# Performance work log

Hardware: AMD Instinct MI355X
Metric: run time of the kernel (lower is better)

The kernel has to match this reference:

```python
import jax, jax.numpy as jnp
import numpy as np


def setup_inputs() -> dict:
    key = jax.random.key(0)
    k0, k1, k2, k3 = jax.random.split(key, 4)
    B, in_dim, n_vars, out_dim, E = 64, 512, 512, 720, 8
    x = jax.random.normal(k0, (B, in_dim, n_vars), dtype=jnp.float32)
    # Gating: nn.Linear(in_dim, E, bias=False) -> weight [E, in_dim]
    Wg = jax.random.normal(k1, (E, in_dim), dtype=jnp.float32) * 0.02
    # Experts: nn.Linear(in_dim, out_dim) -> weight [out_dim, in_dim], bias [out_dim]
    We = jax.random.normal(k2, (E, out_dim, in_dim), dtype=jnp.float32) * 0.02
    be = jax.random.normal(k3, (E, out_dim), dtype=jnp.float32) * 0.02
    return {"x": x, "Wg": Wg, "We": We, "be": be, "top_k": 2}


def reference(x, Wg, We, be, top_k):
    # x: [B, in_len, n_vars] -> tokens along n_vars with feature dim in_len
    xt = jnp.swapaxes(x, 1, 2)                      # [B, V, D]
    gate = jax.nn.softmax(xt @ Wg.T, axis=-1)       # [B, V, E]
    weights, sel = jax.lax.top_k(gate, top_k)       # [B, V, k]
    E, O, D = We.shape
    out = jnp.zeros(xt.shape[:2] + (O,), dtype=xt.dtype)  # [B, V, O]
    for e in range(E):
        # combine weight for expert e: sum over top-k slots routed to e
        coef = jnp.sum(jnp.where(sel == e, weights, jnp.zeros_like(weights)), axis=-1)  # [B, V]
        out = out + coef[..., None] * (jnp.einsum('bvd,od->bvo', xt, We[e]) + be[e])
    return jnp.swapaxes(out, 1, 2)                  # [B, pred_len, n_vars]
```

## Files before the change

kernel.cpp:

```cpp
#include <hip/hip_runtime.h>
#include <hip/hip_bf16.h>

#define DID 512
#define NV  512
#define NB  64
#define OD  720
#define OPAD 768
#define NE  8
#define NTOK (NB * NV)
#define MAXTILE 512

typedef short  bf16x8 __attribute__((ext_vector_type(8)));
typedef float  f32x4  __attribute__((ext_vector_type(4)));

#define XT_OFF    0u
#define WB_OFF    33554432u
#define PID_OFF   39845888u
#define C1D_OFF   39976960u
#define C2D_OFF   40108032u
#define TL_OFF    40239104u
#define CL1_OFF   40370176u
#define CL2_OFF   40501248u
#define BCNT_OFF  40632320u
#define BFILL_OFF 40632576u
#define BOFF_OFF  40632832u
#define TPID_OFF  40633088u
#define TT0_OFF   40635136u
#define TEND_OFF  40637184u
#define NT_OFF    40639232u
#define SCR_OFF   40639488u
#define SCR_END   87825408u

static __device__ __forceinline__ ushort f2bf(float f) {
  unsigned u = __float_as_uint(f);
  unsigned r = (u + 0x7fffu + ((u >> 16) & 1u)) >> 16;
  return (ushort)r;
}
static __device__ __forceinline__ float bf2f(ushort u) {
  return __uint_as_float(((unsigned)u) << 16);
}
static __device__ __forceinline__ void async16(const ushort* g, ushort* l) {
  __builtin_amdgcn_global_load_lds((__attribute__((address_space(1))) void*)(g),
                                   (__attribute__((address_space(3))) void*)(l),
                                   16, 0, 0);
}
static __device__ __forceinline__ int swz(int r) { return (r & 3) ^ ((r >> 2) & 1); }

__global__ __launch_bounds__(512, 4) void k_gatet(const float* __restrict__ x,
                                                  const float* __restrict__ Wg,
                                                  ushort* __restrict__ xt,
                                                  int* __restrict__ pairid,
                                                  float* __restrict__ c1d,
                                                  float* __restrict__ c2d,
                                                  int* __restrict__ bcnt) {
  __shared__ float wg[NE * DID];
  __shared__ float part[8][64][NE + 1];
  __shared__ int cnt64[64];
  const int tid = threadIdx.x;
  for (int i = tid; i < NE * DID / 4; i += 512)
    ((float4*)wg)[i] = ((const float4*)Wg)[i];
  if (tid < 64) cnt64[tid] = 0;
  __syncthreads();

  const int b    = blockIdx.y;
  const int v0   = blockIdx.x * 64;
  const int w    = tid >> 6;
  const int lane = tid & 63;
  const int v    = v0 + lane;
  const int d0   = w * 64;
  const float* xp = x + ((size_t)b * DID + d0) * NV + v;
  ushort* xtp = xt + ((size_t)b * NV + v) * DID + d0;

  float acc[NE];
#pragma unroll
  for (int e = 0; e < NE; ++e) acc[e] = 0.f;

  bf16x8 pk8[8];
  for (int c = 0; c < 64; c += 8) {
    float xv[8];
#pragma unroll
    for (int u = 0; u < 8; ++u) xv[u] = xp[(size_t)(c + u) * NV];
#pragma unroll
    for (int e = 0; e < NE; ++e) {
      const float* wp = &wg[e * DID + d0 + c];
      float4 wa = *(const float4*)wp;
      float4 wb4 = *(const float4*)(wp + 4);
      acc[e] += xv[0] * wa.x + xv[1] * wa.y + xv[2] * wa.z + xv[3] * wa.w
              + xv[4] * wb4.x + xv[5] * wb4.y + xv[6] * wb4.z + xv[7] * wb4.w;
    }
    bf16x8 pk;
#pragma unroll
    for (int u = 0; u < 8; ++u) pk[u] = (short)f2bf(xv[u]);
    pk8[c >> 3] = pk;
  }
#pragma unroll
  for (int ci = 0; ci < 8; ++ci)
    *(bf16x8*)(xtp + ci * 8) = pk8[ci];

#pragma unroll
  for (int e = 0; e < NE; ++e) part[w][lane][e] = acc[e];
  __syncthreads();

  if (tid < 64) {
    float a[NE];
#pragma unroll
    for (int e = 0; e < NE; ++e) {
      float s = part[0][tid][e];
#pragma unroll
      for (int q = 1; q < 8; ++q) s += part[q][tid][e];
      a[e] = s;
    }
    float mx = a[0];
#pragma unroll
    for (int e = 1; e < NE; ++e) mx = fmaxf(mx, a[e]);
    float sum = 0.f;
#pragma unroll
    for (int e = 0; e < NE; ++e) { a[e] = __expf(a[e] - mx); sum += a[e]; }
    const float inv = 1.f / sum;

    int i1 = 0; float g1 = a[0];
#pragma unroll
    for (int e = 1; e < NE; ++e) if (a[e] > g1) { g1 = a[e]; i1 = e; }
    int i2 = -1; float g2 = -1.f;
#pragma unroll
    for (int e = 0; e < NE; ++e) if (e != i1 && a[e] > g2) { g2 = a[e]; i2 = e; }
    g1 *= inv; g2 *= inv;

    int ea, eb; float ca, cb;
    if (i1 < i2) { ea = i1; eb = i2; ca = g1; cb = g2; }
    else         { ea = i2; eb = i1; ca = g2; cb = g1; }
    const int pid = ea * 8 + eb;
    const int t = b * NV + v0 + tid;
    pairid[t] = pid; c1d[t] = ca; c2d[t] = cb;
    atomicAdd(&cnt64[pid], 1);
  }
  __syncthreads();
  if (tid < 64 && cnt64[tid]) atomicAdd(&bcnt[tid], cnt64[tid]);
}

__global__ __launch_bounds__(256) void k_wbconv(const float* __restrict__ We,
                                                ushort* __restrict__ wb) {
  const int e = blockIdx.y;
  const int i = blockIdx.x * 256 + threadIdx.x;
  const int o = i >> 9;
  ushort val = 0;
  if (o < OD) val = f2bf(We[(size_t)e * OD * DID + i]);
  wb[(size_t)e * OPAD * DID + i] = val;
}

__global__ void k_prefix(const int* __restrict__ bcnt, int* __restrict__ boffs,
                         int* __restrict__ tpid, int* __restrict__ tt0,
                         int* __restrict__ tend, int* __restrict__ ntp) {
  const int p = threadIdx.x;
  const int c = bcnt[p];
  int run = c;
#pragma unroll
  for (int s = 1; s < 64; s <<= 1) {
    int up = __shfl_up(run, s, 64);
    if (p >= s) run += up;
  }
  const int excl = run - c;
  boffs[p] = excl;
  const int ntiles = (c + 127) >> 7;
  int trun = ntiles;
#pragma unroll
  for (int s = 1; s < 64; s <<= 1) {
    int up = __shfl_up(trun, s, 64);
    if (p >= s) trun += up;
  }
  const int texcl = trun - ntiles;
  for (int i = 0; i < ntiles; ++i) {
    tpid[texcl + i] = p;
    tt0[texcl + i]  = excl + i * 128;
    tend[texcl + i] = excl + c;
  }
  if (p == 63) ntp[0] = texcl + ntiles;
}

__global__ __launch_bounds__(256) void k_scatter(const int* __restrict__ pairid,
                                                 const float* __restrict__ c1d,
                                                 const float* __restrict__ c2d,
                                                 const int* __restrict__ boffs,
                                                 int* __restrict__ bfill,
                                                 int* __restrict__ tlist,
                                                 float* __restrict__ cl1,
                                                 float* __restrict__ cl2) {
  __shared__ int cnt64[64], base64[64];
  const int tid = threadIdx.x;
  if (tid < 64) cnt64[tid] = 0;
  __syncthreads();
  const int t = blockIdx.x * 256 + tid;
  const int pid = pairid[t];
  const int p = atomicAdd(&cnt64[pid], 1);
  __syncthreads();
  if (tid < 64) base64[tid] = cnt64[tid] ? atomicAdd(&bfill[tid], cnt64[tid]) : 0;
  __syncthreads();
  const int slot = boffs[pid] + base64[pid] + p;
  tlist[slot] = t; cl1[slot] = c1d[t]; cl2[slot] = c2d[t];
}

__global__ __launch_bounds__(256, 2) void k_gemm(
    const ushort* __restrict__ xt, const ushort* __restrict__ wb,
    const float* __restrict__ be, const int* __restrict__ tlist,
    const float* __restrict__ cl1, const float* __restrict__ cl2,
    const int* __restrict__ tpid, const int* __restrict__ tt0,
    const int* __restrict__ tendarr, const int* __restrict__ ntp,
    ushort* __restrict__ scratch, float* __restrict__ out, int mode) {
  const int tile = blockIdx.x;
  if (tile >= ntp[0]) return;
  const int pid  = tpid[tile];
  const int t0   = tt0[tile];
  const int tend = tendarr[tile];
  const int e1 = pid >> 3, e2 = pid & 7;
  const int o0 = blockIdx.y * 256;

  __shared__ __align__(16) ushort As[3][8192];
  __shared__ __align__(16) ushort Bs[3][4096];

  const int tid  = threadIdx.x;
  const int lane = tid & 63;
  const int w    = tid >> 6;

  int aoffA[4];
#pragma unroll
  for (int i = 0; i < 4; ++i) {
    const int f = w * 256 + i * 64 + lane;
    const int r = f >> 2, p = f & 3, q = p ^ swz(r);
    aoffA[i] = (o0 + r) * DID + q * 8;
  }
  int boffB[2];
#pragma unroll
  for (int i = 0; i < 2; ++i) {
    const int f = w * 128 + i * 64 + lane;
    const int r = f >> 2, p = f & 3, q = p ^ swz(r);
    const int sl = t0 + r;
    const int tk = (sl < tend) ? tlist[sl] : 0;
    boffB[i] = tk * DID + q * 8;
  }

  const int m    = lane & 15;
  const int quad = lane >> 4;
  const int wt   = (w & 1) * 64;
  const int wo   = (w >> 1) * 128;

  float ratio[4], c2v[4]; int tokv[4]; bool gv[4];
#pragma unroll
  for (int j = 0; j < 4; ++j) {
    const int sl = t0 + wt + j * 16 + m;
    gv[j] = sl < tend;
    const float cc1 = gv[j] ? cl1[sl] : 0.f;
    const float cc2 = gv[j] ? cl2[sl] : 1.f;
    ratio[j] = cc1 / cc2;
    c2v[j]   = gv[j] ? cc2 : 0.f;
    tokv[j]  = gv[j] ? tlist[sl] : 0;
  }

  f32x4 acc[8][4];
#pragma unroll
  for (int i = 0; i < 8; ++i)
#pragma unroll
    for (int j = 0; j < 4; ++j) acc[i][j] = (f32x4){0.f, 0.f, 0.f, 0.f};

#define STAGE(t, buf) do {                                          \
    const int eA_ = ((t) < 16) ? e1 : e2;                           \
    const int k0_ = ((t) & 15) * 32;                                \
    const ushort* wA_ = wb + (size_t)eA_ * OPAD * DID + k0_;        \
    async16(wA_ + aoffA[0], &As[buf][w * 2048]);                    \
    async16(wA_ + aoffA[1], &As[buf][w * 2048 + 512]);              \
    async16(wA_ + aoffA[2], &As[buf][w * 2048 + 1024]);             \
    async16(wA_ + aoffA[3], &As[buf][w * 2048 + 1536]);             \
    async16(xt + boffB[0] + k0_, &Bs[buf][w * 1024]);               \
    async16(xt + boffB[1] + k0_, &Bs[buf][w * 1024 + 512]);         \
  } while (0)

#define FRAGS(buf)                                                       \
    bf16x8 af[8], bfr[4];                                                \
    {                                                                    \
      const ushort* Asb = &As[buf][0];                                   \
      const ushort* Bsb = &Bs[buf][0];                                   \
      _Pragma("unroll")                                                  \
      for (int i = 0; i < 8; ++i) {                                      \
        const int R = wo + i * 16 + m;                                   \
        af[i] = *(const bf16x8*)(Asb + R * 32 + ((quad ^ swz(R)) << 3)); \
      }                                                                  \
      _Pragma("unroll")                                                  \
      for (int j = 0; j < 4; ++j) {                                      \
        const int R = wt + j * 16 + m;                                   \
        bfr[j] = *(const bf16x8*)(Bsb + R * 32 + ((quad ^ swz(R)) << 3));\
      }                                                                  \
    }

#define MFMA32()                                                         \
    __builtin_amdgcn_s_setprio(1);                                       \
    _Pragma("unroll")                                                    \
    for (int i = 0; i < 8; ++i)                                          \
      _Pragma("unroll")                                                  \
      for (int j = 0; j < 4; ++j)                                        \
        acc[i][j] = __builtin_amdgcn_mfma_f32_16x16x32_bf16(af[i], bfr[j],\
                                                            acc[i][j], 0, 0, 0); \
    __builtin_amdgcn_s_setprio(0);

  STAGE(0, 0);
  STAGE(1, 1);
  STAGE(2, 2);

  int cur = 0;
  for (int kk = 0; kk < 29; ++kk) {
    asm volatile("s_waitcnt vmcnt(12)" ::: "memory");
    __builtin_amdgcn_s_barrier();

    if (kk == 16) {
      const float* be1p = be + e1 * OD;
#pragma unroll
      for (int i = 0; i < 8; ++i) {
        const int ob = o0 + wo + i * 16 + quad * 4;
        float b0 = 0, b1 = 0, b2 = 0, b3 = 0;
        if (ob < OD) { b0 = be1p[ob]; b1 = be1p[ob + 1]; b2 = be1p[ob + 2]; b3 = be1p[ob + 3]; }
#pragma unroll
        for (int j = 0; j < 4; ++j) {
          acc[i][j][0] = (acc[i][j][0] + b0) * ratio[j];
          acc[i][j][1] = (acc[i][j][1] + b1) * ratio[j];
          acc[i][j][2] = (acc[i][j][2] + b2) * ratio[j];
          acc[i][j][3] = (acc[i][j][3] + b3) * ratio[j];
        }
      }
    }

    FRAGS(cur)
    asm volatile("s_waitcnt lgkmcnt(0)" ::: "memory");
    __builtin_amdgcn_s_barrier();
    STAGE(kk + 3, cur);
    MFMA32()
    cur = (cur == 2) ? 0 : cur + 1;
  }

  {
    asm volatile("s_waitcnt vmcnt(12)" ::: "memory");
    __builtin_amdgcn_s_barrier();
    FRAGS(2)
    MFMA32()
  }
  {
    asm volatile("s_waitcnt vmcnt(6)" ::: "memory");
    __builtin_amdgcn_s_barrier();
    FRAGS(0)
    MFMA32()
  }
  {
    asm volatile("s_waitcnt vmcnt(0)" ::: "memory");
    __builtin_amdgcn_s_barrier();
    FRAGS(1)
    MFMA32()
  }

#undef STAGE
#undef FRAGS
#undef MFMA32

  const float* be2p = be + e2 * OD;
#pragma unroll
  for (int i = 0; i < 8; ++i) {
    const int ob = o0 + wo + i * 16 + quad * 4;
    if (ob < OD) {
      const float b0 = be2p[ob], b1 = be2p[ob + 1], b2 = be2p[ob + 2], b3 = be2p[ob + 3];
#pragma unroll
      for (int j = 0; j < 4; ++j) {
        if (gv[j]) {
          const float v0 = c2v[j] * (acc[i][j][0] + b0);
          const float v1 = c2v[j] * (acc[i][j][1] + b1);
          const float v2 = c2v[j] * (acc[i][j][2] + b2);
          const float v3 = c2v[j] * (acc[i][j][3] + b3);
          if (mode == 0) {
            ushort4 pk = make_ushort4(f2bf(v0), f2bf(v1), f2bf(v2), f2bf(v3));
            *(ushort4*)(scratch + (size_t)tokv[j] * OD + ob) = pk;
          } else {
            const int bb = tokv[j] >> 9, vv = tokv[j] & 511;
            float* op = out + ((size_t)bb * OD + ob) * NV + vv;
            op[0] = v0; op[(size_t)NV] = v1; op[2 * (size_t)NV] = v2; op[3 * (size_t)NV] = v3;
          }
        }
      }
    }
  }
}

__global__ __launch_bounds__(256) void k_combine(const ushort* __restrict__ scratch,
                                                 float* __restrict__ out) {
  __shared__ ushort s[64][68];
  const int v0 = blockIdx.x * 64;
  const int o0 = blockIdx.y * 64;
  const int b  = blockIdx.z;
  const int tid = threadIdx.x;
#pragma unroll
  for (int it = 0; it < 2; ++it) {
    const int c = it * 256 + tid;
    const int row = c >> 3, cg = c & 7;
    const int o = o0 + cg * 8;
    if (o + 8 <= OD) {
      const ushort* src = scratch + ((size_t)(b * NV + v0 + row)) * OD + o;
      ushort4 ua = *(const ushort4*)(src);
      ushort4 ub = *(const ushort4*)(src + 4);
      *(ushort4*)&s[row][cg * 8] = ua;
      *(ushort4*)&s[row][cg * 8 + 4] = ub;
    }
  }
  __syncthreads();
  const int vv = tid & 63;
  const int og = tid >> 6;
#pragma unroll
  for (int oi = 0; oi < 8; ++oi) {
    const int ol = (og * 8 + oi) * 2;
    const int o = o0 + ol;
    if (o < OD) {
      ushort2 u = *(const ushort2*)&s[vv][ol];
      float* op = out + ((size_t)b * OD + o) * NV + v0 + vv;
      op[0]  = bf2f(u.x);
      op[NV] = bf2f(u.y);
    }
  }
}

extern "C" void kernel_launch(void* const* d_in, const int* in_sizes, int n_in,
                              void* d_out, int out_size, void* d_ws, size_t ws_size,
                              hipStream_t stream) {
  const float* x  = (const float*)d_in[0];
  const float* Wg = (const float*)d_in[1];
  const float* We = (const float*)d_in[2];
  const float* be = (const float*)d_in[3];
  float* out = (float*)d_out;

  char* ws = (char*)d_ws;
  ushort* xt     = (ushort*)(ws + XT_OFF);
  ushort* wb     = (ushort*)(ws + WB_OFF);
  int*    pairid = (int*)   (ws + PID_OFF);
  float*  c1d    = (float*) (ws + C1D_OFF);
  float*  c2d    = (float*) (ws + C2D_OFF);
  int*    tlist  = (int*)   (ws + TL_OFF);
  float*  cl1    = (float*) (ws + CL1_OFF);
  float*  cl2    = (float*) (ws + CL2_OFF);
  int*    bcnt   = (int*)   (ws + BCNT_OFF);
  int*    bfill  = (int*)   (ws + BFILL_OFF);
  int*    boffs  = (int*)   (ws + BOFF_OFF);
  int*    tpid   = (int*)   (ws + TPID_OFF);
  int*    tt0    = (int*)   (ws + TT0_OFF);
  int*    tend   = (int*)   (ws + TEND_OFF);
  int*    ntp    = (int*)   (ws + NT_OFF);
  ushort* scratch= (ushort*)(ws + SCR_OFF);

  const int mode = (ws_size >= (size_t)SCR_END) ? 0 : 1;

  (void)hipMemsetAsync(bcnt, 0, 512, stream);

  k_gatet<<<dim3(NV / 64, NB), 512, 0, stream>>>(x, Wg, xt, pairid, c1d, c2d, bcnt);
  k_wbconv<<<dim3(OPAD * DID / 256, NE), 256, 0, stream>>>(We, wb);
  k_prefix<<<1, 64, 0, stream>>>(bcnt, boffs, tpid, tt0, tend, ntp);
  k_scatter<<<NTOK / 256, 256, 0, stream>>>(pairid, c1d, c2d, boffs, bfill,
                                            tlist, cl1, cl2);
  k_gemm<<<dim3(320, OPAD / 256), 256, 0, stream>>>(xt, wb, be, tlist, cl1, cl2,
                                                    tpid, tt0, tend, ntp,
                                                    scratch, out, mode);
  if (mode == 0)
    k_combine<<<dim3(NV / 64, (OD + 63) / 64, NB), 256, 0, stream>>>(scratch, out);
}
```

Baseline: 287.8 us.

## Load expert weight fragments directly into registers, bypassing LDS staging

The A operand (expert weights) is no longer staged through a triple-buffered LDS tile. Each wave now loads its 8 MFMA fragments straight from global memory into registers, double-buffered across k-steps (afA/afB), while only the token operand B still goes through async LDS copies. This removes about 48KB of LDS and its read traffic, and waits less on LDS for A. The cost is more VGPR pressure and duplicated A loads across waves that share output rows. The A global loads are also narrower (64B per row per step), and the waitcnt schedule was retuned to match.

```diff
diff --git a/kernel.cpp b/kernel.cpp
--- a/kernel.cpp
+++ b/kernel.cpp
@@ -214,20 +214,12 @@
   const int e1 = pid >> 3, e2 = pid & 7;
   const int o0 = blockIdx.y * 256;
 
-  __shared__ __align__(16) ushort As[3][8192];
   __shared__ __align__(16) ushort Bs[3][4096];
 
   const int tid  = threadIdx.x;
   const int lane = tid & 63;
   const int w    = tid >> 6;
 
-  int aoffA[4];
-#pragma unroll
-  for (int i = 0; i < 4; ++i) {
-    const int f = w * 256 + i * 64 + lane;
-    const int r = f >> 2, p = f & 3, q = p ^ swz(r);
-    aoffA[i] = (o0 + r) * DID + q * 8;
-  }
   int boffB[2];
 #pragma unroll
   for (int i = 0; i < 2; ++i) {
@@ -242,6 +234,13 @@
   const int quad = lane >> 4;
   const int wt   = (w & 1) * 64;
   const int wo   = (w >> 1) * 128;
+
+  int avoff[8];
+#pragma unroll
+  for (int i = 0; i < 8; ++i)
+    avoff[i] = (o0 + wo + i * 16 + m) * DID + quad * 8;
+  const ushort* wbE1 = wb + (size_t)e1 * OPAD * DID;
+  const ushort* wbE2 = wb + (size_t)e2 * OPAD * DID;
 
   float ratio[4], c2v[4]; int tokv[4]; bool gv[4];
 #pragma unroll
@@ -261,101 +260,108 @@
 #pragma unroll
     for (int j = 0; j < 4; ++j) acc[i][j] = (f32x4){0.f, 0.f, 0.f, 0.f};
 
-#define STAGE(t, buf) do {                                          \
-    const int eA_ = ((t) < 16) ? e1 : e2;                           \
+  bf16x8 afA[8], afB[8], bfr[4];
+
+#define STAGE_B(t, buf) do {                                        \
     const int k0_ = ((t) & 15) * 32;                                \
-    const ushort* wA_ = wb + (size_t)eA_ * OPAD * DID + k0_;        \
-    async16(wA_ + aoffA[0], &As[buf][w * 2048]);                    \
-    async16(wA_ + aoffA[1], &As[buf][w * 2048 + 512]);              \
-    async16(wA_ + aoffA[2], &As[buf][w * 2048 + 1024]);             \
-    async16(wA_ + aoffA[3], &As[buf][w * 2048 + 1536]);             \
     async16(xt + boffB[0] + k0_, &Bs[buf][w * 1024]);               \
     async16(xt + boffB[1] + k0_, &Bs[buf][w * 1024 + 512]);         \
   } while (0)
 
-#define FRAGS(buf)                                                       \
-    bf16x8 af[8], bfr[4];                                                \
-    {                                                                    \
-      const ushort* Asb = &As[buf][0];                                   \
-      const ushort* Bsb = &Bs[buf][0];                                   \
-      _Pragma("unroll")                                                  \
-      for (int i = 0; i < 8; ++i) {                                      \
-        const int R = wo + i * 16 + m;                                   \
-        af[i] = *(const bf16x8*)(Asb + R * 32 + ((quad ^ swz(R)) << 3)); \
-      }                                                                  \
-      _Pragma("unroll")                                                  \
-      for (int j = 0; j < 4; ++j) {                                      \
-        const int R = wt + j * 16 + m;                                   \
-        bfr[j] = *(const bf16x8*)(Bsb + R * 32 + ((quad ^ swz(R)) << 3));\
-      }                                                                  \
-    }
-
-#define MFMA32()                                                         \
-    __builtin_amdgcn_s_setprio(1);                                       \
-    _Pragma("unroll")                                                    \
-    for (int i = 0; i < 8; ++i)                                          \
-      _Pragma("unroll")                                                  \
-      for (int j = 0; j < 4; ++j)                                        \
-        acc[i][j] = __builtin_amdgcn_mfma_f32_16x16x32_bf16(af[i], bfr[j],\
-                                                            acc[i][j], 0, 0, 0); \
+#define ALOAD(t, AF) do {                                           \
+    const ushort* abase_ = (((t) < 16) ? wbE1 : wbE2) + ((t) & 15) * 32; \
+    _Pragma("unroll")                                               \
+    for (int i_ = 0; i_ < 8; ++i_)                                  \
+      AF[i_] = *(const bf16x8*)(abase_ + avoff[i_]);                \
+  } while (0)
+
+#define FRAGS_B(buf) do {                                           \
+    const ushort* Bsb = &Bs[0][0] + (buf) * 4096;                   \
+    _Pragma("unroll")                                               \
+    for (int j_ = 0; j_ < 4; ++j_) {                                \
+      const int R = wt + j_ * 16 + m;                               \
+      bfr[j_] = *(const bf16x8*)(Bsb + R * 32 + ((quad ^ swz(R)) << 3)); \
+    }                                                               \
+  } while (0)
+
+#define MFMA32(AF)                                                  \
+    __builtin_amdgcn_s_setprio(1);                                  \
+    _Pragma("unroll")                                               \
+    for (int i_ = 0; i_ < 8; ++i_)                                  \
+      _Pragma("unroll")                                             \
+      for (int j_ = 0; j_ < 4; ++j_)                                \
+        acc[i_][j_] = __builtin_amdgcn_mfma_f32_16x16x32_bf16(AF[i_], bfr[j_], \
+                                                              acc[i_][j_], 0, 0, 0); \
     __builtin_amdgcn_s_setprio(0);
 
-  STAGE(0, 0);
-  STAGE(1, 1);
-  STAGE(2, 2);
-
-  int cur = 0;
-  for (int kk = 0; kk < 29; ++kk) {
-    asm volatile("s_waitcnt vmcnt(12)" ::: "memory");
+#define FOLD(kk) if ((kk) == 16) {                                  \
+    const float* be1p = be + e1 * OD;                               \
+    _Pragma("unroll")                                               \
+    for (int i_ = 0; i_ < 8; ++i_) {                                \
+      const int ob = o0 + wo + i_ * 16 + quad * 4;                  \
+      float b0 = 0, b1 = 0, b2 = 0, b3 = 0;                         \
+      if (ob < OD) { b0 = be1p[ob]; b1 = be1p[ob + 1];              \
+                     b2 = be1p[ob + 2]; b3 = be1p[ob + 3]; }        \
+      _Pragma("unroll")                                             \
+      for (int j_ = 0; j_ < 4; ++j_) {                              \
+        acc[i_][j_][0] = (acc[i_][j_][0] + b0) * ratio[j_];         \
+        acc[i_][j_][1] = (acc[i_][j_][1] + b1) * ratio[j_];         \
+        acc[i_][j_][2] = (acc[i_][j_][2] + b2) * ratio[j_];         \
+        acc[i_][j_][3] = (acc[i_][j_][3] + b3) * ratio[j_];         \
+      }                                                             \
+    }                                                               \
+  }
+
+#define KSTEP(kk, AFU, AFL) do {                                    \
+    asm volatile("s_waitcnt vmcnt(10)" ::: "memory");               \
+    __builtin_amdgcn_s_barrier();                                   \
+    FOLD(kk)                                                        \
+    ALOAD((kk) + 1, AFL);                                           \
+    FRAGS_B((kk) % 3);                                              \
+    asm volatile("s_waitcnt lgkmcnt(0)" ::: "memory");              \
+    __builtin_amdgcn_s_barrier();                                   \
+    STAGE_B((kk) + 3, (kk) % 3);                                    \
+    MFMA32(AFU)                                                     \
+  } while (0)
+
+  STAGE_B(0, 0);
+  STAGE_B(1, 1);
+  STAGE_B(2, 2);
+  ALOAD(0, afA);
+
+  for (int kk = 0; kk < 28; kk += 2) {
+    KSTEP(kk, afA, afB);
+    KSTEP(kk + 1, afB, afA);
+  }
+  KSTEP(28, afA, afB);
+
+  {
+    asm volatile("s_waitcnt vmcnt(10)" ::: "memory");
     __builtin_amdgcn_s_barrier();
-
-    if (kk == 16) {
-      const float* be1p = be + e1 * OD;
-#pragma unroll
-      for (int i = 0; i < 8; ++i) {
-        const int ob = o0 + wo + i * 16 + quad * 4;
-        float b0 = 0, b1 = 0, b2 = 0, b3 = 0;
-        if (ob < OD) { b0 = be1p[ob]; b1 = be1p[ob + 1]; b2 = be1p[ob + 2]; b3 = be1p[ob + 3]; }
-#pragma unroll
-        for (int j = 0; j < 4; ++j) {
-          acc[i][j][0] = (acc[i][j][0] + b0) * ratio[j];
-          acc[i][j][1] = (acc[i][j][1] + b1) * ratio[j];
-          acc[i][j][2] = (acc[i][j][2] + b2) * ratio[j];
-          acc[i][j][3] = (acc[i][j][3] + b3) * ratio[j];
-        }
-      }
-    }
-
-    FRAGS(cur)
-    asm volatile("s_waitcnt lgkmcnt(0)" ::: "memory");
+    ALOAD(30, afA);
+    FRAGS_B(2);
+    MFMA32(afB)
+  }
+  {
+    asm volatile("s_waitcnt vmcnt(10)" ::: "memory");
     __builtin_amdgcn_s_barrier();
-    STAGE(kk + 3, cur);
-    MFMA32()
-    cur = (cur == 2) ? 0 : cur + 1;
-  }
-
+    ALOAD(31, afB);
+    FRAGS_B(0);
+    MFMA32(afA)
+  }
   {
-    asm volatile("s_waitcnt vmcnt(12)" ::: "memory");
+    asm volatile("s_waitcnt vmcnt(10)" ::: "memory");
     __builtin_amdgcn_s_barrier();
-    FRAGS(2)
-    MFMA32()
-  }
-  {
-    asm volatile("s_waitcnt vmcnt(6)" ::: "memory");
-    __builtin_amdgcn_s_barrier();
-    FRAGS(0)
-    MFMA32()
-  }
-  {
-    asm volatile("s_waitcnt vmcnt(0)" ::: "memory");
-    __builtin_amdgcn_s_barrier();
-    FRAGS(1)
-    MFMA32()
-  }
-
-#undef STAGE
-#undef FRAGS
+    FRAGS_B(1);
+    MFMA32(afB)
+  }
+
+#undef STAGE_B
+#undef ALOAD
+#undef FRAGS_B
 #undef MFMA32
+#undef FOLD
+#undef KSTEP
 
   const float* be2p = be + e2 * OD;
 #pragma unroll
```

New measurement: 383.2 us. 1.33x slower.
